# Kernel tuning notes

Hardware: AMD Instinct MI355X
Metric: run time of the kernel (lower is better)

## Reference

```python
import jax, jax.numpy as jnp
import numpy as np


def setup_inputs() -> dict:
    key = jax.random.key(0)
    ks = jax.random.split(key, 5)
    B, n_sites, d_bond, d_phys = 8192, 2048, 8, 2
    sr = n_sites // 2  # single_rank
    x = jax.random.normal(ks[0], (B, n_sites, d_phys), dtype=jnp.float32)
    scale = 0.01
    left_b = scale * jax.random.normal(ks[1], (d_bond, d_phys), dtype=jnp.float32)
    left = scale * jax.random.normal(ks[2], (sr - 1, d_bond, d_bond, d_phys), dtype=jnp.float32)
    right = scale * jax.random.normal(ks[3], (sr - 1, d_bond, d_bond, d_phys), dtype=jnp.float32)
    right_b = scale * jax.random.normal(ks[4], (d_bond, d_phys), dtype=jnp.float32)
    return {"x": x, "left_b": left_b, "left": left, "right": right, "right_b": right_b}


def reference(x, left_b, left, right, right_b):
    # x: [B, n_sites, d_phys]; left/right: [sr-1, bond, bond, d_phys]; boundaries: [bond, d_phys]
    n_sites = x.shape[1]
    sr = n_sites // 2

    # In-place slice normalizations performed at the top of call()
    left_b = left_b.at[2].set(left_b[2] / jnp.linalg.norm(left_b[2]))
    left = left.at[3].set(left[3] / jnp.linalg.norm(left[3]))
    right = right.at[3].set(right[3] / jnp.linalg.norm(right[3]))
    right_b = right_b.at[2].set(right_b[2] / jnp.linalg.norm(right_b[2]))

    # Left half: boundary phys contraction -> [B, bond]
    lvec = jnp.einsum("ap,kp->ka", left_b, x[:, 0])
    # Middle left: contract site-stack and phys axes -> [B, bond, bond]
    Lmat = jnp.einsum("sabp,ksp->kab", left, x[:, 1:sr])
    l = jnp.einsum("ka,kab->kb", lvec, Lmat)  # contract lb_n[0]^ln[1]

    # Right half (mirror)
    rvec = jnp.einsum("ap,kp->ka", right_b, x[:, n_sites - 1])
    Rmat = jnp.einsum("sabp,ksp->kab", right, x[:, sr : n_sites - 1])
    r = jnp.einsum("ka,kab->kb", rvec, Rmat)

    # Join halves: ln[2]^rn[2] -> scalar per sample, shape [B]
    return jnp.einsum("kb,kb->k", l, r)
```

## Files before the change

kernel.cpp:

```cpp
#include <hip/hip_runtime.h>
#include <hip/hip_bf16.h>

typedef __bf16  bf16x8  __attribute__((ext_vector_type(8)));
typedef float   floatx4 __attribute__((ext_vector_type(4)));

#define ROWLEN      4096
#define B_SAMPLES   8192

typedef const __attribute__((address_space(1))) void* gas1_t;
typedef __attribute__((address_space(3))) void*       las3_t;

__device__ __forceinline__ void stage16(const float* g, float* l) {
    __builtin_amdgcn_global_load_lds((gas1_t)g, (las3_t)l, 16, 0, 0);
}


__global__ __launch_bounds__(256) void repack_kernel(
    const float* __restrict__ left, const float* __restrict__ right,
    __bf16* __restrict__ wfrag)
{
    __shared__ float norms[2];
    const int tid  = threadIdx.x;
    const int wv   = tid >> 6;
    const int ln   = tid & 63;

    if (wv < 2) {
        const float* W = (wv == 0) ? left : right;
        float a = W[384 + ln], b = W[384 + 64 + ln];
        float s = a * a + b * b;
        s += __shfl_xor(s, 1);  s += __shfl_xor(s, 2);  s += __shfl_xor(s, 4);
        s += __shfl_xor(s, 8);  s += __shfl_xor(s, 16); s += __shfl_xor(s, 32);
        if (ln == 0) norms[wv] = 1.0f / sqrtf(s);
    }
    __syncthreads();
    const float invL = norms[0];
    const float invR = norms[1];

    const int g    = (int)(blockIdx.x * 256) + tid;
    const int lane = g & 63;
    const int nt   = (g >> 6) & 3;
    const int t    = (g >> 8) & 63;
    const int h    = (g >> 14) & 1;
    const int kk0  = t * 32 + (lane >> 4) * 8;
    const int n    = nt * 16 + (lane & 15);
    const int a    = n >> 3, bb = n & 7;
    const float* W = (h == 0) ? left : right;

    bf16x8 frag;
#pragma unroll
    for (int si = 0; si < 4; ++si) {
        const int kk = kk0 + si * 2;
        int s;  bool valid;
        if (h == 0) { s = (kk >> 1) - 1; valid = (kk >= 2); }
        else        { s = (kk >> 1);     valid = (s < 1023); }
        float w0 = 0.f, w1 = 0.f;
        if (valid) {
            const float* wp = W + ((s * 8 + a) * 8 + bb) * 2;
            w0 = wp[0]; w1 = wp[1];
            if (s == 3) { const float sc = (h == 0) ? invL : invR; w0 *= sc; w1 *= sc; }
        }
        frag[si * 2]     = (__bf16)w0;
        frag[si * 2 + 1] = (__bf16)w1;
    }
    ((bf16x8*)wfrag)[g] = frag;
}

__global__ __launch_bounds__(512, 2) void mps_main_kernel(
    const float* __restrict__ x, const __bf16* __restrict__ wfrag,
    const float* __restrict__ left_b, const float* __restrict__ right_b,
    float* __restrict__ out)
{
    __shared__ float smem[32768];
    const int tid  = threadIdx.x;
    const int wid  = tid >> 6;
    const int lane = tid & 63;
    const int hw   = wid & 1;
    const int v    = wid >> 1;
    const int mcol = lane & 15;
    const int q    = lane >> 4;
    const int p    = lane & 7;
    const int blk  = blockIdx.x;

    const float* xblk = x + (size_t)blk * 32 * ROWLEN;

#pragma unroll
    for (int i = 0; i < 4; ++i) {
        const int r = 4 * wid + i;
        const float* gp = xblk + (size_t)r * ROWLEN + ((lane ^ (r & 7)) * 4);
        stage16(gp,       &smem[r * 512]);
        stage16(gp + 256, &smem[r * 512 + 256]);
    }
    __syncthreads();

    floatx4 accA0 = {0.f,0.f,0.f,0.f}, accA1 = {0.f,0.f,0.f,0.f};
    floatx4 accA2 = {0.f,0.f,0.f,0.f}, accA3 = {0.f,0.f,0.f,0.f};
    floatx4 accB0 = {0.f,0.f,0.f,0.f}, accB1 = {0.f,0.f,0.f,0.f};
    floatx4 accB2 = {0.f,0.f,0.f,0.f}, accB3 = {0.f,0.f,0.f,0.f};

#pragma unroll
    for (int ch = 0; ch < 8; ++ch) {
        const int cbuf = (ch & 1) * 16384;
        if (ch < 7) {
            const int cn     = ch + 1;
            const int coloff = (cn & 1) * 2048 + (cn >> 1) * 512;
            const int nbuf   = (cn & 1) * 16384;
#pragma unroll
            for (int i = 0; i < 4; ++i) {
                const int r = 4 * wid + i;
                const float* gp = xblk + (size_t)r * ROWLEN + coloff
                                + ((lane ^ (r & 7)) * 4);
                stage16(gp,       &smem[nbuf + r * 512]);
                stage16(gp + 256, &smem[nbuf + r * 512 + 256]);
            }
        }
        if ((ch & 1) == hw) {
            const int cc = ch >> 1;
            const float* sA = &smem[cbuf + mcol * 512];
            const float* sB = &smem[cbuf + (16 + mcol) * 512];
            const bf16x8* bp0 = (const bf16x8*)wfrag
                + ((size_t)((hw * 64 + cc * 16 + 4 * v) * 4)) * 64 + lane;
#pragma unroll
            for (int ti = 0; ti < 4; ++ti) {
                const int g0 = (4 * v + ti) * 8 + 2 * q;
                const floatx4 a0 = *(const floatx4*)&sA[((g0    ) ^ p) * 4];
                const floatx4 a1 = *(const floatx4*)&sA[((g0 + 1) ^ p) * 4];
                const floatx4 b0 = *(const floatx4*)&sB[((g0    ) ^ p) * 4];
                const floatx4 b1 = *(const floatx4*)&sB[((g0 + 1) ^ p) * 4];
                bf16x8 af0, af1;
                af0[0] = (__bf16)a0[0]; af0[1] = (__bf16)a0[1];
                af0[2] = (__bf16)a0[2]; af0[3] = (__bf16)a0[3];
                af0[4] = (__bf16)a1[0]; af0[5] = (__bf16)a1[1];
                af0[6] = (__bf16)a1[2]; af0[7] = (__bf16)a1[3];
                af1[0] = (__bf16)b0[0]; af1[1] = (__bf16)b0[1];
                af1[2] = (__bf16)b0[2]; af1[3] = (__bf16)b0[3];
                af1[4] = (__bf16)b1[0]; af1[5] = (__bf16)b1[1];
                af1[6] = (__bf16)b1[2]; af1[7] = (__bf16)b1[3];
                const bf16x8* bp = bp0 + (size_t)ti * 256;
                const bf16x8 w0 = bp[0], w1 = bp[64], w2 = bp[128], w3 = bp[192];
                accA0 = __builtin_amdgcn_mfma_f32_16x16x32_bf16(af0, w0, accA0, 0, 0, 0);
                accB0 = __builtin_amdgcn_mfma_f32_16x16x32_bf16(af1, w0, accB0, 0, 0, 0);
                accA1 = __builtin_amdgcn_mfma_f32_16x16x32_bf16(af0, w1, accA1, 0, 0, 0);
                accB1 = __builtin_amdgcn_mfma_f32_16x16x32_bf16(af1, w1, accB1, 0, 0, 0);
                accA2 = __builtin_amdgcn_mfma_f32_16x16x32_bf16(af0, w2, accA2, 0, 0, 0);
                accB2 = __builtin_amdgcn_mfma_f32_16x16x32_bf16(af1, w2, accB2, 0, 0, 0);
                accA3 = __builtin_amdgcn_mfma_f32_16x16x32_bf16(af0, w3, accA3, 0, 0, 0);
                accB3 = __builtin_amdgcn_mfma_f32_16x16x32_bf16(af1, w3, accB3, 0, 0, 0);
            }
        }
        __syncthreads();
    }

    {
        const int base = (hw * 4 + v) * 32;
#pragma unroll
        for (int i = 0; i < 4; ++i) {
            const int r0 = q * 4 + i;
            smem[(base + r0) * 65 +  0 + mcol] = accA0[i];
            smem[(base + r0) * 65 + 16 + mcol] = accA1[i];
            smem[(base + r0) * 65 + 32 + mcol] = accA2[i];
            smem[(base + r0) * 65 + 48 + mcol] = accA3[i];
            smem[(base + 16 + r0) * 65 +  0 + mcol] = accB0[i];
            smem[(base + 16 + r0) * 65 + 16 + mcol] = accB1[i];
            smem[(base + 16 + r0) * 65 + 32 + mcol] = accB2[i];
            smem[(base + 16 + r0) * 65 + 48 + mcol] = accB3[i];
        }
    }
    __syncthreads();

    if (tid < 256) {
        const int mm = tid >> 3;
        const int b  = tid & 7;
        const size_t k = (size_t)blk * 32 + mm;
        const float* xr = x + k * ROWLEN;
        const float x0 = xr[0],    x1 = xr[1];
        const float y0 = xr[4094], y1 = xr[4095];
        const float lbn = 1.0f / sqrtf(left_b[4]*left_b[4] + left_b[5]*left_b[5]);
        const float rbn = 1.0f / sqrtf(right_b[4]*right_b[4] + right_b[5]*right_b[5]);
        float l = 0.f, r = 0.f;
#pragma unroll
        for (int a = 0; a < 8; ++a) {
            float lv = left_b[a*2]  * x0 + left_b[a*2+1]  * x1;
            float rv = right_b[a*2] * y0 + right_b[a*2+1] * y1;
            if (a == 2) { lv *= lbn; rv *= rbn; }
            const int n = a * 8 + b;
            const float ls = smem[((0*4+0)*32 + mm)*65 + n] + smem[((0*4+1)*32 + mm)*65 + n]
                           + smem[((0*4+2)*32 + mm)*65 + n] + smem[((0*4+3)*32 + mm)*65 + n];
            const float rs = smem[((1*4+0)*32 + mm)*65 + n] + smem[((1*4+1)*32 + mm)*65 + n]
                           + smem[((1*4+2)*32 + mm)*65 + n] + smem[((1*4+3)*32 + mm)*65 + n];
            l += lv * ls;
            r += rv * rs;
        }
        float vv = l * r;
        vv += __shfl_xor(vv, 1);
        vv += __shfl_xor(vv, 2);
        vv += __shfl_xor(vv, 4);
        if (b == 0) out[k] = vv;
    }
}

extern "C" void kernel_launch(void* const* d_in, const int* in_sizes, int n_in,
                              void* d_out, int out_size, void* d_ws, size_t ws_size,
                              hipStream_t stream)
{
    const float* x       = (const float*)d_in[0];
    const float* left_b  = (const float*)d_in[1];
    const float* left    = (const float*)d_in[2];
    const float* right   = (const float*)d_in[3];
    const float* right_b = (const float*)d_in[4];

    __bf16* wfrag = (__bf16*)d_ws;
    float*  out   = (float*)d_out;

    hipLaunchKernelGGL(repack_kernel, dim3(128), dim3(256), 0, stream,
                       left, right, wfrag);
    hipLaunchKernelGGL(mps_main_kernel, dim3(B_SAMPLES / 32), dim3(512), 0, stream,
                       x, wfrag, left_b, right_b, out);
}
```

Measured before the change: 214.4 us.

## Split work by sample half instead of chain half and hand-schedule waitcnt pipeline

Waves are now assigned to one 16-row half of the sample tile and process every chunk, where before each wave handled all 32 rows on alternate chunks. Weight fragments are loaded into registers at the top of each chunk. Manual vmcnt waits with raw s_barrier replace __syncthreads so the next chunk's LDS staging overlaps the current MFMA work. The intent is to keep every wave busy on each chunk and hide global latency, at the cost of more weight register pressure and fragile hand-written waitcnt counts.

```diff
diff --git a/kernel.cpp b/kernel.cpp
--- a/kernel.cpp
+++ b/kernel.cpp
@@ -74,7 +74,7 @@
     const int tid  = threadIdx.x;
     const int wid  = tid >> 6;
     const int lane = tid & 63;
-    const int hw   = wid & 1;
+    const int AB   = wid & 1;
     const int v    = wid >> 1;
     const int mcol = lane & 15;
     const int q    = lane >> 4;
@@ -90,16 +90,28 @@
         stage16(gp,       &smem[r * 512]);
         stage16(gp + 256, &smem[r * 512 + 256]);
     }
-    __syncthreads();
-
-    floatx4 accA0 = {0.f,0.f,0.f,0.f}, accA1 = {0.f,0.f,0.f,0.f};
-    floatx4 accA2 = {0.f,0.f,0.f,0.f}, accA3 = {0.f,0.f,0.f,0.f};
-    floatx4 accB0 = {0.f,0.f,0.f,0.f}, accB1 = {0.f,0.f,0.f,0.f};
-    floatx4 accB2 = {0.f,0.f,0.f,0.f}, accB3 = {0.f,0.f,0.f,0.f};
+
+    floatx4 accL[4] = {{0.f,0.f,0.f,0.f},{0.f,0.f,0.f,0.f},
+                       {0.f,0.f,0.f,0.f},{0.f,0.f,0.f,0.f}};
+    floatx4 accR[4] = {{0.f,0.f,0.f,0.f},{0.f,0.f,0.f,0.f},
+                       {0.f,0.f,0.f,0.f},{0.f,0.f,0.f,0.f}};
 
 #pragma unroll
     for (int ch = 0; ch < 8; ++ch) {
+        const int h    = ch & 1;
+        const int c    = ch >> 1;
         const int cbuf = (ch & 1) * 16384;
+
+        bf16x8 w[4][4];
+        const bf16x8* bp0 = (const bf16x8*)wfrag
+            + ((size_t)((h * 64 + c * 16 + 4 * v) * 4)) * 64 + lane;
+#pragma unroll
+        for (int ti = 0; ti < 4; ++ti)
+#pragma unroll
+            for (int nt = 0; nt < 4; ++nt)
+                w[ti][nt] = bp0[(size_t)ti * 256 + nt * 64];
+        __builtin_amdgcn_sched_barrier(0);
+
         if (ch < 7) {
             const int cn     = ch + 1;
             const int coloff = (cn & 1) * 2048 + (cn >> 1) * 512;
@@ -112,58 +124,49 @@
                 stage16(gp,       &smem[nbuf + r * 512]);
                 stage16(gp + 256, &smem[nbuf + r * 512 + 256]);
             }
-        }
-        if ((ch & 1) == hw) {
-            const int cc = ch >> 1;
-            const float* sA = &smem[cbuf + mcol * 512];
-            const float* sB = &smem[cbuf + (16 + mcol) * 512];
-            const bf16x8* bp0 = (const bf16x8*)wfrag
-                + ((size_t)((hw * 64 + cc * 16 + 4 * v) * 4)) * 64 + lane;
+            __builtin_amdgcn_sched_barrier(0);
+            asm volatile("s_waitcnt vmcnt(8)" ::: "memory");
+        } else {
+            __builtin_amdgcn_sched_barrier(0);
+            asm volatile("s_waitcnt vmcnt(0)" ::: "memory");
+        }
+        __builtin_amdgcn_s_barrier();
+        __builtin_amdgcn_sched_barrier(0);
+
+        {
+            floatx4* acc = (h == 0) ? accL : accR;
+            const float* sA = &smem[cbuf + (16 * AB + mcol) * 512];
 #pragma unroll
             for (int ti = 0; ti < 4; ++ti) {
                 const int g0 = (4 * v + ti) * 8 + 2 * q;
                 const floatx4 a0 = *(const floatx4*)&sA[((g0    ) ^ p) * 4];
                 const floatx4 a1 = *(const floatx4*)&sA[((g0 + 1) ^ p) * 4];
-                const floatx4 b0 = *(const floatx4*)&sB[((g0    ) ^ p) * 4];
-                const floatx4 b1 = *(const floatx4*)&sB[((g0 + 1) ^ p) * 4];
-                bf16x8 af0, af1;
-                af0[0] = (__bf16)a0[0]; af0[1] = (__bf16)a0[1];
-                af0[2] = (__bf16)a0[2]; af0[3] = (__bf16)a0[3];
-                af0[4] = (__bf16)a1[0]; af0[5] = (__bf16)a1[1];
-                af0[6] = (__bf16)a1[2]; af0[7] = (__bf16)a1[3];
-                af1[0] = (__bf16)b0[0]; af1[1] = (__bf16)b0[1];
-                af1[2] = (__bf16)b0[2]; af1[3] = (__bf16)b0[3];
-                af1[4] = (__bf16)b1[0]; af1[5] = (__bf16)b1[1];
-                af1[6] = (__bf16)b1[2]; af1[7] = (__bf16)b1[3];
-                const bf16x8* bp = bp0 + (size_t)ti * 256;
-                const bf16x8 w0 = bp[0], w1 = bp[64], w2 = bp[128], w3 = bp[192];
-                accA0 = __builtin_amdgcn_mfma_f32_16x16x32_bf16(af0, w0, accA0, 0, 0, 0);
-                accB0 = __builtin_amdgcn_mfma_f32_16x16x32_bf16(af1, w0, accB0, 0, 0, 0);
-                accA1 = __builtin_amdgcn_mfma_f32_16x16x32_bf16(af0, w1, accA1, 0, 0, 0);
-                accB1 = __builtin_amdgcn_mfma_f32_16x16x32_bf16(af1, w1, accB1, 0, 0, 0);
-                accA2 = __builtin_amdgcn_mfma_f32_16x16x32_bf16(af0, w2, accA2, 0, 0, 0);
-                accB2 = __builtin_amdgcn_mfma_f32_16x16x32_bf16(af1, w2, accB2, 0, 0, 0);
-                accA3 = __builtin_amdgcn_mfma_f32_16x16x32_bf16(af0, w3, accA3, 0, 0, 0);
-                accB3 = __builtin_amdgcn_mfma_f32_16x16x32_bf16(af1, w3, accB3, 0, 0, 0);
+                bf16x8 af;
+                af[0] = (__bf16)a0[0]; af[1] = (__bf16)a0[1];
+                af[2] = (__bf16)a0[2]; af[3] = (__bf16)a0[3];
+                af[4] = (__bf16)a1[0]; af[5] = (__bf16)a1[1];
+                af[6] = (__bf16)a1[2]; af[7] = (__bf16)a1[3];
+                acc[0] = __builtin_amdgcn_mfma_f32_16x16x32_bf16(af, w[ti][0], acc[0], 0, 0, 0);
+                acc[1] = __builtin_amdgcn_mfma_f32_16x16x32_bf16(af, w[ti][1], acc[1], 0, 0, 0);
+                acc[2] = __builtin_amdgcn_mfma_f32_16x16x32_bf16(af, w[ti][2], acc[2], 0, 0, 0);
+                acc[3] = __builtin_amdgcn_mfma_f32_16x16x32_bf16(af, w[ti][3], acc[3], 0, 0, 0);
             }
         }
-        __syncthreads();
-    }
-
-    {
-        const int base = (hw * 4 + v) * 32;
-#pragma unroll
-        for (int i = 0; i < 4; ++i) {
-            const int r0 = q * 4 + i;
-            smem[(base + r0) * 65 +  0 + mcol] = accA0[i];
-            smem[(base + r0) * 65 + 16 + mcol] = accA1[i];
-            smem[(base + r0) * 65 + 32 + mcol] = accA2[i];
-            smem[(base + r0) * 65 + 48 + mcol] = accA3[i];
-            smem[(base + 16 + r0) * 65 +  0 + mcol] = accB0[i];
-            smem[(base + 16 + r0) * 65 + 16 + mcol] = accB1[i];
-            smem[(base + 16 + r0) * 65 + 32 + mcol] = accB2[i];
-            smem[(base + 16 + r0) * 65 + 48 + mcol] = accB3[i];
-        }
+        __builtin_amdgcn_sched_barrier(0);
+        __builtin_amdgcn_s_barrier();
+    }
+
+#pragma unroll
+    for (int i = 0; i < 4; ++i) {
+        const int row = 16 * AB + q * 4 + i;
+        smem[((0 * 4 + v) * 32 + row) * 65 +  0 + mcol] = accL[0][i];
+        smem[((0 * 4 + v) * 32 + row) * 65 + 16 + mcol] = accL[1][i];
+        smem[((0 * 4 + v) * 32 + row) * 65 + 32 + mcol] = accL[2][i];
+        smem[((0 * 4 + v) * 32 + row) * 65 + 48 + mcol] = accL[3][i];
+        smem[((1 * 4 + v) * 32 + row) * 65 +  0 + mcol] = accR[0][i];
+        smem[((1 * 4 + v) * 32 + row) * 65 + 16 + mcol] = accR[1][i];
+        smem[((1 * 4 + v) * 32 + row) * 65 + 32 + mcol] = accR[2][i];
+        smem[((1 * 4 + v) * 32 + row) * 65 + 48 + mcol] = accR[3][i];
     }
     __syncthreads();
 
```

After: 207.0 us. 3.5% less time.
